# Kernel tuning notes

Hardware: AMD Instinct MI355X
Metric: run time of the kernel (lower is better)

## Reference

```python
import jax, jax.numpy as jnp
import numpy as np

B, CO, P = 4, 80, 9          # batch, out_channels, point_num
HI, WI = 128, 128            # input feature-map size
HO, WO = 128, 128            # output (location) spatial size


def setup_inputs() -> dict:
    key = jax.random.key(0)
    k1, k2, k3 = jax.random.split(key, 3)
    x = jax.random.normal(k1, (B, P * CO, HI, WI), jnp.float32)
    # location holds absolute (y, x) coords, interleaved per point: 2*P channels
    loc = jax.random.uniform(k2, (B, 2 * P, HO, WO), jnp.float32) * (HI - 1)
    bias = jax.random.normal(k3, (CO,), jnp.float32) * 0.01
    return {"x": x, "location": loc, "bias": bias}


def _collect_merge(x, location, bias):
    Bn, Cin, Hi, Wi = x.shape
    Pn = location.shape[1] // 2
    Ho, Wo = location.shape[2], location.shape[3]
    Co = Cin // Pn  # channels_offset == out_channels
    feat = x.reshape(Bn, Pn, Co, Hi * Wi)           # [B,P,Co,Hi*Wi]
    loc = location.reshape(Bn, Pn, 2, Ho, Wo)
    y, xc = loc[:, :, 0], loc[:, :, 1]              # [B,P,Ho,Wo]
    y0 = jnp.floor(y)
    x0 = jnp.floor(xc)
    dy, dx = y - y0, xc - x0
    y0i = y0.astype(jnp.int32)
    x0i = x0.astype(jnp.int32)
    out = jnp.zeros((Bn, Pn, Co, Ho * Wo), x.dtype)
    taps = [(0, 0, (1 - dy) * (1 - dx)), (0, 1, (1 - dy) * dx),
            (1, 0, dy * (1 - dx)), (1, 1, dy * dx)]
    for oy, ox, w in taps:  # 4 bilinear taps (fixed small loop)
        yi = y0i + oy
        xi = x0i + ox
        valid = (yi >= 0) & (yi < Hi) & (xi >= 0) & (xi < Wi)
        idx = (jnp.clip(yi, 0, Hi - 1) * Wi + jnp.clip(xi, 0, Wi - 1))
        idx = idx.reshape(Bn, Pn, 1, Ho * Wo)
        tap = jnp.take_along_axis(
            feat, jnp.broadcast_to(idx, (Bn, Pn, Co, Ho * Wo)), axis=3)
        out = out + tap * (w * valid).reshape(Bn, Pn, 1, Ho * Wo)
    # merge (sum over point_num) + per-channel bias
    out = out.sum(axis=1).reshape(Bn, Co, Ho, Wo) + bias[None, :, None, None]
    return out


def reference(x, location, bias):
    return _collect_merge(x, location, bias)
```

## Files before the change

### kernel.cpp

```cpp
#include <hip/hip_runtime.h>
#include <cstddef>
#include <cstdint>

constexpr int B_  = 4;
constexpr int CO_ = 80;
constexpr int PN_ = 9;
constexpr int HI_ = 128;
constexpr int WI_ = 128;
constexpr int HW_ = HI_ * WI_;

__global__ __launch_bounds__(256) void transpose_bf16_k(const float* __restrict__ x,
                                                        uint16_t* __restrict__ xt) {
    const int bp  = blockIdx.y;
    const int hw0 = blockIdx.x << 6;

    __shared__ uint16_t tile[CO_][65];

    const float* src = x + (size_t)bp * CO_ * HW_ + hw0;
    for (int i = threadIdx.x; i < CO_ * 64; i += 256) {
        const int co  = i >> 6;
        const int hwl = i & 63;
        const uint32_t u = __float_as_uint(src[(size_t)co * HW_ + hwl]);
        const uint32_t r = (u + 0x7fffu + ((u >> 16) & 1u)) >> 16;
        tile[co][hwl] = (uint16_t)r;
    }
    __syncthreads();

    uint32_t* dst = (uint32_t*)(xt + ((size_t)bp * HW_ + hw0) * CO_);
    for (int i = threadIdx.x; i < 64 * (CO_ / 2); i += 256) {
        const int hwl = i / 40;
        const int cp  = i - hwl * 40;
        const uint32_t lo = tile[2 * cp][hwl];
        const uint32_t hi = tile[2 * cp + 1][hwl];
        dst[hwl * 40 + cp] = lo | (hi << 16);
    }
}

__global__ __launch_bounds__(320) void gather_bf16_k(const uint16_t* __restrict__ xt,
                                                     const float* __restrict__ loc,
                                                     const float* __restrict__ bias,
                                                     float* __restrict__ out) {
    const int b   = blockIdx.x >> 9;
    const int hw0 = (blockIdx.x & 511) << 5;
    const int tid = threadIdx.x;

    __shared__ float wts[PN_][32][4];
    __shared__ int   idxs[PN_][32][4];
    __shared__ float accs[32][CO_ + 1];

    if (tid < PN_ * 32) {
        const int p    = tid >> 5;
        const int pixl = tid & 31;
        const float y = loc[(((size_t)b * PN_ + p) * 2 + 0) * HW_ + hw0 + pixl];
        const float x = loc[(((size_t)b * PN_ + p) * 2 + 1) * HW_ + hw0 + pixl];
        const float y0f = floorf(y), x0f = floorf(x);
        const int   y0 = (int)y0f,  x0 = (int)x0f;
        const float dy = y - y0f,   dx = x - x0f;
        const float w[4] = { (1.f - dy) * (1.f - dx), (1.f - dy) * dx,
                             dy * (1.f - dx),         dy * dx };
#pragma unroll
        for (int c = 0; c < 4; ++c) {
            const int yi = y0 + (c >> 1);
            const int xi = x0 + (c & 1);
            const bool valid = (yi >= 0) & (yi < HI_) & (xi >= 0) & (xi < WI_);
            const int yc = min(max(yi, 0), HI_ - 1);
            const int xc = min(max(xi, 0), WI_ - 1);
            wts[p][pixl][c]  = valid ? w[c] : 0.f;
            idxs[p][pixl][c] = yc * WI_ + xc;
        }
    }
    __syncthreads();

    const int pixl = tid / 10;
    const int cg   = tid - pixl * 10;

    float acc[8];
#pragma unroll
    for (int j = 0; j < 8; ++j) acc[j] = bias[cg * 8 + j];

    for (int p = 0; p < PN_; ++p) {
        const uint16_t* base = xt + ((size_t)b * PN_ + p) * (size_t)HW_ * CO_;
#pragma unroll
        for (int c = 0; c < 4; ++c) {
            const int   idx = idxs[p][pixl][c];
            const float w   = wts[p][pixl][c];
            const uint4 v = *(const uint4*)((const uint32_t*)(base + (size_t)idx * CO_) + cg * 4);
            const uint32_t us[4] = { v.x, v.y, v.z, v.w };
#pragma unroll
            for (int j = 0; j < 4; ++j) {
                const float f0 = __uint_as_float(us[j] << 16);
                const float f1 = __uint_as_float(us[j] & 0xffff0000u);
                acc[2 * j]     = fmaf(f0, w, acc[2 * j]);
                acc[2 * j + 1] = fmaf(f1, w, acc[2 * j + 1]);
            }
        }
    }

#pragma unroll
    for (int j = 0; j < 8; ++j) accs[pixl][cg * 8 + j] = acc[j];
    __syncthreads();

    for (int i = tid; i < 32 * CO_; i += 320) {
        const int co  = i >> 5;
        const int hwl = i & 31;
        out[((size_t)b * CO_ + co) * HW_ + hw0 + hwl] = accs[hwl][co];
    }
}

__global__ __launch_bounds__(256) void gather_direct_k(const float* __restrict__ xsrc,
                                                       const float* __restrict__ loc,
                                                       const float* __restrict__ bias,
                                                       float* __restrict__ out) {
    const int b   = blockIdx.x >> 10;
    const int hw0 = (blockIdx.x & 1023) << 4;
    const int tid = threadIdx.x;

    __shared__ float wts[PN_][16][4];
    __shared__ int   idxs[PN_][16][4];
    __shared__ float accs[16][CO_ + 1];

    if (tid < PN_ * 16) {
        const int p    = tid >> 4;
        const int pixl = tid & 15;
        const float y = loc[(((size_t)b * PN_ + p) * 2 + 0) * HW_ + hw0 + pixl];
        const float x = loc[(((size_t)b * PN_ + p) * 2 + 1) * HW_ + hw0 + pixl];
        const float y0f = floorf(y), x0f = floorf(x);
        const int   y0 = (int)y0f,  x0 = (int)x0f;
        const float dy = y - y0f,   dx = x - x0f;
        const float w[4] = { (1.f - dy) * (1.f - dx), (1.f - dy) * dx,
                             dy * (1.f - dx),         dy * dx };
#pragma unroll
        for (int c = 0; c < 4; ++c) {
            const int yi = y0 + (c >> 1);
            const int xi = x0 + (c & 1);
            const bool valid = (yi >= 0) & (yi < HI_) & (xi >= 0) & (xi < WI_);
            const int yc = min(max(yi, 0), HI_ - 1);
            const int xc = min(max(xi, 0), WI_ - 1);
            wts[p][pixl][c]  = valid ? w[c] : 0.f;
            idxs[p][pixl][c] = yc * WI_ + xc;
        }
    }
    __syncthreads();

    float myacc[5];
    int   cos[5], pixls[5];
#pragma unroll
    for (int k = 0; k < 5; ++k) {
        const int item = tid + (k << 8);
        const int pixl = item / CO_;
        const int co   = item - pixl * CO_;
        cos[k] = co; pixls[k] = pixl;
        myacc[k] = bias[co];
    }
    for (int p = 0; p < PN_; ++p) {
        const float* base = xsrc + ((size_t)b * PN_ + p) * CO_ * HW_;
#pragma unroll
        for (int k = 0; k < 5; ++k) {
#pragma unroll
            for (int c = 0; c < 4; ++c) {
                const int   idx = idxs[p][pixls[k]][c];
                const float w   = wts[p][pixls[k]][c];
                myacc[k] = fmaf(base[(size_t)cos[k] * HW_ + idx], w, myacc[k]);
            }
        }
    }
#pragma unroll
    for (int k = 0; k < 5; ++k) accs[pixls[k]][cos[k]] = myacc[k];
    __syncthreads();
    for (int i = tid; i < 16 * CO_; i += 256) {
        const int co  = i >> 4;
        const int hwl = i & 15;
        out[((size_t)b * CO_ + co) * HW_ + hw0 + hwl] = accs[hwl][co];
    }
}

extern "C" void kernel_launch(void* const* d_in, const int* in_sizes, int n_in,
                              void* d_out, int out_size, void* d_ws, size_t ws_size,
                              hipStream_t stream) {
    const float* x    = (const float*)d_in[0];
    const float* loc  = (const float*)d_in[1];
    const float* bias = (const float*)d_in[2];
    float*       out  = (float*)d_out;

    const size_t need = (size_t)B_ * PN_ * CO_ * HW_ * sizeof(uint16_t);
    if (ws_size >= need) {
        uint16_t* xt = (uint16_t*)d_ws;
        dim3 g1(HW_ / 64, B_ * PN_);
        transpose_bf16_k<<<g1, 256, 0, stream>>>(x, xt);
        gather_bf16_k<<<dim3(B_ * HW_ / 32), 320, 0, stream>>>(xt, loc, bias, out);
    } else {
        gather_direct_k<<<dim3(B_ * HW_ / 16), 256, 0, stream>>>(x, loc, bias, out);
    }
}
```

Before: 111.7 us.

## Vectorize bf16 transpose and process two pixels per thread in gather

The transpose kernel now handles 128 pixels per block, reading float4 and writing uint4 packed bf16 rows so that global loads and stores are wider. The gather kernel covers 64 pixels per block, with each thread accumulating two pixels and issuing eight 16-byte gathers before doing the math, which gives more memory-level parallelism. Precomputed byte offsets and a shared-memory union keep LDS usage in check. In exchange, register pressure rises and there are half as many blocks, which may lower occupancy.

```diff
diff --git a/kernel.cpp b/kernel.cpp
--- a/kernel.cpp
+++ b/kernel.cpp
@@ -9,30 +9,42 @@
 constexpr int WI_ = 128;
 constexpr int HW_ = HI_ * WI_;
 
+__device__ __forceinline__ uint16_t f2bf(float f) {
+    uint32_t u = __float_as_uint(f);
+    return (uint16_t)((u + 0x7fffu + ((u >> 16) & 1u)) >> 16);
+}
+
 __global__ __launch_bounds__(256) void transpose_bf16_k(const float* __restrict__ x,
                                                         uint16_t* __restrict__ xt) {
     const int bp  = blockIdx.y;
-    const int hw0 = blockIdx.x << 6;
-
-    __shared__ uint16_t tile[CO_][65];
+    const int hw0 = blockIdx.x << 7;
+
+    __shared__ uint16_t tile[CO_][136];
 
     const float* src = x + (size_t)bp * CO_ * HW_ + hw0;
-    for (int i = threadIdx.x; i < CO_ * 64; i += 256) {
-        const int co  = i >> 6;
-        const int hwl = i & 63;
-        const uint32_t u = __float_as_uint(src[(size_t)co * HW_ + hwl]);
-        const uint32_t r = (u + 0x7fffu + ((u >> 16) & 1u)) >> 16;
-        tile[co][hwl] = (uint16_t)r;
+    for (int i = threadIdx.x; i < CO_ * 32; i += 256) {
+        const int co = i >> 5;
+        const int h4 = (i & 31) << 2;
+        const float4 v = *(const float4*)(src + (size_t)co * HW_ + h4);
+        ushort4 pk;
+        pk.x = f2bf(v.x); pk.y = f2bf(v.y); pk.z = f2bf(v.z); pk.w = f2bf(v.w);
+        *(ushort4*)&tile[co][h4] = pk;
     }
     __syncthreads();
 
     uint32_t* dst = (uint32_t*)(xt + ((size_t)bp * HW_ + hw0) * CO_);
-    for (int i = threadIdx.x; i < 64 * (CO_ / 2); i += 256) {
-        const int hwl = i / 40;
-        const int cp  = i - hwl * 40;
-        const uint32_t lo = tile[2 * cp][hwl];
-        const uint32_t hi = tile[2 * cp + 1][hwl];
-        dst[hwl * 40 + cp] = lo | (hi << 16);
+    for (int i = threadIdx.x; i < 128 * 10; i += 256) {
+        const int px = i / 10;
+        const int cp = i - px * 10;
+        uint4 wv;
+        uint32_t* w = (uint32_t*)&wv;
+#pragma unroll
+        for (int j = 0; j < 4; ++j) {
+            const uint32_t lo = tile[cp * 8 + 2 * j][px];
+            const uint32_t hi = tile[cp * 8 + 2 * j + 1][px];
+            w[j] = lo | (hi << 16);
+        }
+        *(uint4*)(dst + px * 40 + cp * 4) = wv;
     }
 }
 
@@ -40,17 +52,18 @@
                                                      const float* __restrict__ loc,
                                                      const float* __restrict__ bias,
                                                      float* __restrict__ out) {
-    const int b   = blockIdx.x >> 9;
-    const int hw0 = (blockIdx.x & 511) << 5;
+    const int b   = blockIdx.x >> 8;
+    const int hw0 = (blockIdx.x & 255) << 6;
     const int tid = threadIdx.x;
 
-    __shared__ float wts[PN_][32][4];
-    __shared__ int   idxs[PN_][32][4];
-    __shared__ float accs[32][CO_ + 1];
-
-    if (tid < PN_ * 32) {
-        const int p    = tid >> 5;
-        const int pixl = tid & 31;
+    __shared__ union SM {
+        struct { float w[PN_][64][4]; int off[PN_][64][4]; } ab;
+        float accs[64][81];
+    } sm;
+
+    for (int item = tid; item < PN_ * 64; item += 320) {
+        const int p    = item >> 6;
+        const int pixl = item & 63;
         const float y = loc[(((size_t)b * PN_ + p) * 2 + 0) * HW_ + hw0 + pixl];
         const float x = loc[(((size_t)b * PN_ + p) * 2 + 1) * HW_ + hw0 + pixl];
         const float y0f = floorf(y), x0f = floorf(x);
@@ -65,45 +78,61 @@
             const bool valid = (yi >= 0) & (yi < HI_) & (xi >= 0) & (xi < WI_);
             const int yc = min(max(yi, 0), HI_ - 1);
             const int xc = min(max(xi, 0), WI_ - 1);
-            wts[p][pixl][c]  = valid ? w[c] : 0.f;
-            idxs[p][pixl][c] = yc * WI_ + xc;
-        }
-    }
-    __syncthreads();
-
-    const int pixl = tid / 10;
-    const int cg   = tid - pixl * 10;
-
-    float acc[8];
-#pragma unroll
-    for (int j = 0; j < 8; ++j) acc[j] = bias[cg * 8 + j];
+            sm.ab.w[p][pixl][c]   = valid ? w[c] : 0.f;
+            sm.ab.off[p][pixl][c] = (yc * WI_ + xc) * (CO_ * 2);
+        }
+    }
+    __syncthreads();
+
+    const int px0 = tid / 10;
+    const int cg  = tid - px0 * 10;
+    const int px1 = px0 + 32;
+
+    float acc0[8], acc1[8];
+#pragma unroll
+    for (int j = 0; j < 8; ++j) { acc0[j] = bias[cg * 8 + j]; acc1[j] = acc0[j]; }
 
     for (int p = 0; p < PN_; ++p) {
-        const uint16_t* base = xt + ((size_t)b * PN_ + p) * (size_t)HW_ * CO_;
-#pragma unroll
-        for (int c = 0; c < 4; ++c) {
-            const int   idx = idxs[p][pixl][c];
-            const float w   = wts[p][pixl][c];
-            const uint4 v = *(const uint4*)((const uint32_t*)(base + (size_t)idx * CO_) + cg * 4);
-            const uint32_t us[4] = { v.x, v.y, v.z, v.w };
+        const char* base = (const char*)(xt + ((size_t)b * PN_ + p) * (size_t)HW_ * CO_)
+                           + cg * 16;
+        uint4 v0[4], v1[4];
+        float w0[4], w1[4];
+#pragma unroll
+        for (int c = 0; c < 4; ++c) {
+            v0[c] = *(const uint4*)(base + sm.ab.off[p][px0][c]);
+            w0[c] = sm.ab.w[p][px0][c];
+        }
+#pragma unroll
+        for (int c = 0; c < 4; ++c) {
+            v1[c] = *(const uint4*)(base + sm.ab.off[p][px1][c]);
+            w1[c] = sm.ab.w[p][px1][c];
+        }
+#pragma unroll
+        for (int c = 0; c < 4; ++c) {
+            const uint32_t* u0 = (const uint32_t*)&v0[c];
+            const uint32_t* u1 = (const uint32_t*)&v1[c];
 #pragma unroll
             for (int j = 0; j < 4; ++j) {
-                const float f0 = __uint_as_float(us[j] << 16);
-                const float f1 = __uint_as_float(us[j] & 0xffff0000u);
-                acc[2 * j]     = fmaf(f0, w, acc[2 * j]);
-                acc[2 * j + 1] = fmaf(f1, w, acc[2 * j + 1]);
+                acc0[2*j]   = fmaf(__uint_as_float(u0[j] << 16),        w0[c], acc0[2*j]);
+                acc0[2*j+1] = fmaf(__uint_as_float(u0[j] & 0xffff0000u), w0[c], acc0[2*j+1]);
+                acc1[2*j]   = fmaf(__uint_as_float(u1[j] << 16),        w1[c], acc1[2*j]);
+                acc1[2*j+1] = fmaf(__uint_as_float(u1[j] & 0xffff0000u), w1[c], acc1[2*j+1]);
             }
         }
     }
 
-#pragma unroll
-    for (int j = 0; j < 8; ++j) accs[pixl][cg * 8 + j] = acc[j];
-    __syncthreads();
-
-    for (int i = tid; i < 32 * CO_; i += 320) {
-        const int co  = i >> 5;
-        const int hwl = i & 31;
-        out[((size_t)b * CO_ + co) * HW_ + hw0 + hwl] = accs[hwl][co];
+    __syncthreads();
+#pragma unroll
+    for (int j = 0; j < 8; ++j) {
+        sm.accs[px0][cg * 8 + j] = acc0[j];
+        sm.accs[px1][cg * 8 + j] = acc1[j];
+    }
+    __syncthreads();
+
+    for (int i = tid; i < 64 * CO_; i += 320) {
+        const int co  = i >> 6;
+        const int hwl = i & 63;
+        out[((size_t)b * CO_ + co) * HW_ + hw0 + hwl] = sm.accs[hwl][co];
     }
 }
 
@@ -185,9 +214,9 @@
     const size_t need = (size_t)B_ * PN_ * CO_ * HW_ * sizeof(uint16_t);
     if (ws_size >= need) {
         uint16_t* xt = (uint16_t*)d_ws;
-        dim3 g1(HW_ / 64, B_ * PN_);
+        dim3 g1(HW_ / 128, B_ * PN_);
         transpose_bf16_k<<<g1, 256, 0, stream>>>(x, xt);
-        gather_bf16_k<<<dim3(B_ * HW_ / 32), 320, 0, stream>>>(xt, loc, bias, out);
+        gather_bf16_k<<<dim3(B_ * HW_ / 64), 320, 0, stream>>>(xt, loc, bias, out);
     } else {
         gather_direct_k<<<dim3(B_ * HW_ / 16), 256, 0, stream>>>(x, loc, bias, out);
     }
```

Result: slower. 115.8 us (+3.7%).
